# Kernel optimization log

Measured on AMD Instinct MI355X. Metric: run time of the kernel, lower is better.

Reference implementation:

```python
import jax, jax.numpy as jnp
import numpy as np

# DualAttention dims
D_MODEL = 1024
H_SA = 8          # self-attention heads
H_RA = 8          # relational-attention heads
TOTAL_H = H_SA + H_RA
HEAD_DIM = D_MODEL // TOTAL_H   # 64
KEY_DIM = HEAD_DIM              # 64
N_REL = 8
REL_PROJ = HEAD_DIM * H_RA // N_REL  # 64
B, S = 2, 2048


def apply_rope(x, cos, sin):
    # x: [b, s, h, d]; cos/sin: [s, d//2]. Pairs are (0,1),(2,3),... as in
    # llama-style apply_rotary_emb (reshape(..., -1, 2).unbind(-1)).
    xr, xi = x[..., 0::2], x[..., 1::2]
    c = cos[None, :, None, :]
    s_ = sin[None, :, None, :]
    out = jnp.stack([xr * c - xi * s_, xr * s_ + xi * c], axis=-1)
    return out.reshape(x.shape)


def setup_inputs() -> dict:
    key = jax.random.key(0)
    ks = jax.random.split(key, 16)
    def w(k, shape):
        return jax.random.normal(k, shape, jnp.float32) * 0.02
    x = jax.random.normal(ks[0], (B, S, D_MODEL), jnp.float32)
    symbols = jax.random.normal(ks[1], (B, S, D_MODEL), jnp.float32)
    # real RoPE tables
    pos = np.arange(S, dtype=np.float32)[:, None]
    inv = 1.0 / (10000.0 ** (np.arange(0, KEY_DIM, 2, dtype=np.float32) / KEY_DIM))
    ang = pos * inv[None, :]
    freqs_cos = jnp.asarray(np.cos(ang), jnp.float32)
    freqs_sin = jnp.asarray(np.sin(ang), jnp.float32)
    return dict(
        x=x, symbols=symbols, freqs_cos=freqs_cos, freqs_sin=freqs_sin,
        # self-attention branch (torch Linear weights: [out, in])
        wq_sa=w(ks[2], (H_SA * KEY_DIM, D_MODEL)),
        wk_sa=w(ks[3], (H_SA * KEY_DIM, D_MODEL)),
        wv_sa=w(ks[4], (H_SA * HEAD_DIM, D_MODEL)),
        wo_sa=w(ks[5], (H_SA * HEAD_DIM, H_SA * HEAD_DIM)),
        # relational-attention branch
        wq_attn=w(ks[6], (H_RA * KEY_DIM, D_MODEL)),
        wk_attn=w(ks[7], (H_RA * KEY_DIM, D_MODEL)),
        wq_rel=w(ks[8], (N_REL * REL_PROJ, D_MODEL)),
        wk_rel=w(ks[9], (N_REL * REL_PROJ, D_MODEL)),
        wr=w(ks[10], (H_RA, HEAD_DIM, N_REL)),
        wv_ra=w(ks[11], (H_RA * HEAD_DIM, D_MODEL)),
        wo_ra=w(ks[12], (H_RA * HEAD_DIM, H_RA * HEAD_DIM)),
    )


def reference(x, symbols, freqs_cos, freqs_sin,
              wq_sa, wk_sa, wv_sa, wo_sa,
              wq_attn, wk_attn, wq_rel, wk_rel, wr, wv_ra, wo_ra):
    b, s, _ = x.shape
    attn_scale = 1.0 / np.sqrt(HEAD_DIM).astype(np.float32)
    rel_scale = 1.0 / np.sqrt(REL_PROJ).astype(np.float32)
    causal = jnp.tril(jnp.ones((s, s), dtype=bool))
    neg = jnp.finfo(x.dtype).min

    def heads(t, h, d):
        return t.reshape(b, s, h, d)

    # ---- self-attention branch (causal SDPA with RoPE) ----
    q = apply_rope(heads(x @ wq_sa.T, H_SA, KEY_DIM), freqs_cos, freqs_sin)
    k = apply_rope(heads(x @ wk_sa.T, H_SA, KEY_DIM), freqs_cos, freqs_sin)
    v = heads(x @ wv_sa.T, H_SA, HEAD_DIM)
    scores = jnp.einsum('bihd,bjhd->bhij', q, k) * attn_scale
    a = jax.nn.softmax(jnp.where(causal, scores, neg), axis=-1)
    sa_out = jnp.einsum('bhij,bjhd->bihd', a, v).reshape(b, s, H_SA * HEAD_DIM) @ wo_sa.T

    # ---- relational-attention branch ----
    # attention scores (softmax selection), with RoPE
    qa = apply_rope(heads(x @ wq_attn.T, H_RA, KEY_DIM), freqs_cos, freqs_sin)
    ka = apply_rope(heads(x @ wk_attn.T, H_RA, KEY_DIM), freqs_cos, freqs_sin)
    ra_scores = jnp.einsum('bihd,bjhd->bhij', qa, ka) * attn_scale
    alpha = jax.nn.softmax(jnp.where(causal, ra_scores, neg), axis=-1)
    # relations r(x_i, x_j) in R^{N_REL} (identity rel_activation)
    qr = heads(x @ wq_rel.T, N_REL, REL_PROJ)
    kr = heads(x @ wk_rel.T, N_REL, REL_PROJ)
    rel = jnp.einsum('birp,bjrp->brij', qr, kr) * rel_scale  # [b, R, i, j]
    # symbol values: wv applied to retrieved symbols
    sv = heads(symbols @ wv_ra.T, H_RA, HEAD_DIM)
    attended_sym = jnp.einsum('bhij,bjhd->bihd', alpha, sv)          # [b, i, h, d]
    attended_rel = jnp.einsum('bhij,brij->bihr', alpha, rel)         # [b, i, h, R]
    rel_out = jnp.einsum('bihr,hdr->bihd', attended_rel, wr)
    ra_out = (attended_sym + rel_out).reshape(b, s, H_RA * HEAD_DIM) @ wo_ra.T

    # DualAttention: concat branch outputs along feature dim -> [b, s, d_model]
    return jnp.concatenate([sa_out, ra_out], axis=-1)
```

## Files before the change

kernel.cpp:

```cpp
#include <hip/hip_runtime.h>

#define B_   2
#define S_   2048
#define H_   8
#define D_   64
#define DM_  1024
#define PJ_  512
#define NT_  32
#define NTRI 528
#define NCHK 80

typedef short bf16x8 __attribute__((ext_vector_type(8)));
typedef float f32x4 __attribute__((ext_vector_type(4)));

__device__ __forceinline__ float bf2f(unsigned int u) {
  return __uint_as_float(u << 16);
}
__device__ __forceinline__ unsigned short f2bf(float f) {
  unsigned int u = __float_as_uint(f);
  u += 0x7fffu + ((u >> 16) & 1u);
  return (unsigned short)(u >> 16);
}

struct CvtJobs {
  const float*    src[12];
  unsigned short* dst[12];
  int             n4[12];
};

__global__ __launch_bounds__(256) void cvt_many(CvtJobs J) {
  const int j = blockIdx.y;
  const int i = blockIdx.x * 256 + threadIdx.x;
  if (i >= J.n4[j]) return;
  const float4 v = ((const float4*)J.src[j])[i];
  ushort4 o;
  o.x = f2bf(v.x); o.y = f2bf(v.y); o.z = f2bf(v.z); o.w = f2bf(v.w);
  ((ushort4*)J.dst[j])[i] = o;
}

template <int KD, typename CT>
__device__ __forceinline__
void gemm128_body(const unsigned short* __restrict__ A, int m0,
                  const unsigned short* __restrict__ Wb,
                  CT* __restrict__ Cb, int ldc,
                  unsigned short* As, unsigned short* Bs)
{
  const int tid = threadIdx.x;
  const int wv = tid >> 6, lane = tid & 63;
  const int r15 = lane & 15, quad = lane >> 4;
  const int wm = (wv >> 1) * 64, wn = (wv & 1) * 64;
  f32x4 acc[4][4];
#pragma unroll
  for (int i = 0; i < 4; ++i)
#pragma unroll
    for (int j = 0; j < 4; ++j) acc[i][j] = (f32x4){0.f, 0.f, 0.f, 0.f};

  const int srow = tid >> 1;
  const int sc2  = (tid & 1) * 2;
  const unsigned short* ga = A + (size_t)(m0 + srow) * KD + sc2 * 8;
  const unsigned short* gb = Wb + (size_t)srow * KD + sc2 * 8;
  unsigned short* la = As + srow * 40 + sc2 * 8;
  unsigned short* lb = Bs + srow * 40 + sc2 * 8;

  for (int kk = 0; kk < KD; kk += 32) {
    __syncthreads();
    const uint4 a0 = *(const uint4*)(ga + kk);
    const uint4 a1 = *(const uint4*)(ga + kk + 8);
    const uint4 b0 = *(const uint4*)(gb + kk);
    const uint4 b1 = *(const uint4*)(gb + kk + 8);
    *(uint4*)la       = a0;
    *(uint4*)(la + 8) = a1;
    *(uint4*)lb       = b0;
    *(uint4*)(lb + 8) = b1;
    __syncthreads();
    bf16x8 af[4], bf[4];
#pragma unroll
    for (int i = 0; i < 4; ++i)
      af[i] = *(const bf16x8*)(As + (wm + i * 16 + r15) * 40 + quad * 8);
#pragma unroll
    for (int j = 0; j < 4; ++j)
      bf[j] = *(const bf16x8*)(Bs + (wn + j * 16 + r15) * 40 + quad * 8);
#pragma unroll
    for (int i = 0; i < 4; ++i)
#pragma unroll
      for (int j = 0; j < 4; ++j)
        acc[i][j] = __builtin_amdgcn_mfma_f32_16x16x32_bf16(af[i], bf[j], acc[i][j], 0, 0, 0);
  }
#pragma unroll
  for (int i = 0; i < 4; ++i)
#pragma unroll
    for (int r = 0; r < 4; ++r) {
      CT* cp = Cb + (size_t)(wm + i * 16 + quad * 4 + r) * ldc + wn + r15;
#pragma unroll
      for (int j = 0; j < 4; ++j) {
        if constexpr (sizeof(CT) == 2) cp[j * 16] = f2bf(acc[i][j][r]);
        else                           cp[j * 16] = acc[i][j][r];
      }
    }
}

__global__ __launch_bounds__(256)
void proj_tiled(const unsigned short* __restrict__ XB,
                const unsigned short* __restrict__ SYB,
                const unsigned short* __restrict__ Wcat,
                unsigned short* __restrict__ Qbase,
                unsigned short* __restrict__ SV)
{
  __shared__ unsigned short As[128 * 40];
  __shared__ unsigned short Bs[128 * 40];
  const int m0 = blockIdx.x * 128;
  const int ny = blockIdx.y;
  const size_t NB = (size_t)B_ * S_ * PJ_;
  const unsigned short* A;
  const unsigned short* Wb;
  unsigned short* Cb;
  if (ny < 28) {
    const int n0 = ny * 128;
    A  = XB;
    Wb = Wcat + (size_t)n0 * DM_;
    Cb = Qbase + (size_t)(n0 >> 9) * NB + (size_t)m0 * PJ_ + (n0 & 511);
  } else {
    const int n0 = (ny - 28) * 128;
    A  = SYB;
    Wb = Wcat + (size_t)7 * PJ_ * DM_ + (size_t)n0 * DM_;
    Cb = SV + (size_t)m0 * PJ_ + n0;
  }
  gemm128_body<DM_, unsigned short>(A, m0, Wb, Cb, PJ_, As, Bs);
}

__global__ __launch_bounds__(256)
void out_tiled(const unsigned short* __restrict__ Asa,
               const unsigned short* __restrict__ Ara,
               const unsigned short* __restrict__ WOSA,
               const unsigned short* __restrict__ WORA,
               float* __restrict__ Out)
{
  __shared__ unsigned short As[128 * 40];
  __shared__ unsigned short Bs[64 * 40];
  const int m0 = blockIdx.x * 128;
  const int ny = blockIdx.y;
  const int n0 = (ny & 7) * 64;
  const unsigned short* A  = (ny < 8) ? Asa : Ara;
  const unsigned short* Wb = ((ny < 8) ? WOSA : WORA) + (size_t)n0 * PJ_;
  float* Cb = Out + (size_t)m0 * DM_ + ((ny < 8) ? 0 : 512) + n0;

  const int tid = threadIdx.x;
  const int wv = tid >> 6, lane = tid & 63;
  const int r15 = lane & 15, quad = lane >> 4;
  const int wm = wv * 32;
  f32x4 acc[2][4];
#pragma unroll
  for (int i = 0; i < 2; ++i)
#pragma unroll
    for (int j = 0; j < 4; ++j) acc[i][j] = (f32x4){0.f, 0.f, 0.f, 0.f};

  const int arow = tid >> 1, ac = (tid & 1) * 16;
  const int brow = tid >> 2, bc = (tid & 3) * 8;
  const unsigned short* ga = A + (size_t)(m0 + arow) * PJ_ + ac;
  const unsigned short* gb = Wb + (size_t)brow * PJ_ + bc;
  unsigned short* la = As + arow * 40 + ac;
  unsigned short* lb = Bs + brow * 40 + bc;

  for (int kk = 0; kk < PJ_; kk += 32) {
    __syncthreads();
    const uint4 a0 = *(const uint4*)(ga + kk);
    const uint4 a1 = *(const uint4*)(ga + kk + 8);
    const uint4 b0 = *(const uint4*)(gb + kk);
    *(uint4*)la       = a0;
    *(uint4*)(la + 8) = a1;
    *(uint4*)lb       = b0;
    __syncthreads();
    bf16x8 af[2], bf[4];
#pragma unroll
    for (int i = 0; i < 2; ++i)
      af[i] = *(const bf16x8*)(As + (wm + i * 16 + r15) * 40 + quad * 8);
#pragma unroll
    for (int j = 0; j < 4; ++j)
      bf[j] = *(const bf16x8*)(Bs + (j * 16 + r15) * 40 + quad * 8);
#pragma unroll
    for (int i = 0; i < 2; ++i)
#pragma unroll
      for (int j = 0; j < 4; ++j)
        acc[i][j] = __builtin_amdgcn_mfma_f32_16x16x32_bf16(af[i], bf[j], acc[i][j], 0, 0, 0);
  }
#pragma unroll
  for (int i = 0; i < 2; ++i)
#pragma unroll
    for (int r = 0; r < 4; ++r) {
      float* cp = Cb + (size_t)(wm + i * 16 + quad * 4 + r) * DM_ + r15;
#pragma unroll
      for (int j = 0; j < 4; ++j) cp[j * 16] = acc[i][j][r];
    }
}

__global__ __launch_bounds__(256)
void rel_gemm(const unsigned short* __restrict__ QRg, const unsigned short* __restrict__ KRg,
              unsigned short* __restrict__ RelCF)
{
  __shared__ unsigned short As[128 * 72];
  __shared__ unsigned short Bs[128 * 72];
  const int t = blockIdx.x;
  int I = 0;
  while ((I + 1) * (I + 2) / 2 <= t) ++I;
  const int J = t - I * (I + 1) / 2;
  const int rr = blockIdx.y & 7, b = blockIdx.y >> 3;
  const int tid = threadIdx.x;
  const int wv = tid >> 6, lane = tid & 63;
  const int r15 = lane & 15, quad = lane >> 4;

  const int srow = tid >> 1, c32 = (tid & 1) * 32;
  const unsigned short* ga = QRg + (size_t)(b * S_ + I * 128 + srow) * PJ_ + rr * 64 + c32;
  const unsigned short* gb = KRg + (size_t)(b * S_ + J * 128 + srow) * PJ_ + rr * 64 + c32;
  unsigned short* la = As + srow * 72 + c32;
  unsigned short* lb = Bs + srow * 72 + c32;
#pragma unroll
  for (int q = 0; q < 4; ++q) {
    *(uint4*)(la + q * 8) = *(const uint4*)(ga + q * 8);
    *(uint4*)(lb + q * 8) = *(const uint4*)(gb + q * 8);
  }
  __syncthreads();

  const int wm = (wv >> 1) * 64, wn = (wv & 1) * 64;
  const int it64 = 2 * I + (wv >> 1), jt64 = 2 * J + (wv & 1);
  if (jt64 > it64) return;
  f32x4 acc[4][4];
#pragma unroll
  for (int i = 0; i < 4; ++i)
#pragma unroll
    for (int j = 0; j < 4; ++j) acc[i][j] = (f32x4){0.f, 0.f, 0.f, 0.f};
#pragma unroll
  for (int k0 = 0; k0 < 2; ++k0) {
    bf16x8 af[4], bf[4];
#pragma unroll
    for (int i = 0; i < 4; ++i)
      af[i] = *(const bf16x8*)(As + (wm + i * 16 + r15) * 72 + quad * 8 + k0 * 32);
#pragma unroll
    for (int j = 0; j < 4; ++j)
      bf[j] = *(const bf16x8*)(Bs + (wn + j * 16 + r15) * 72 + quad * 8 + k0 * 32);
#pragma unroll
    for (int i = 0; i < 4; ++i)
#pragma unroll
      for (int j = 0; j < 4; ++j)
        acc[i][j] = __builtin_amdgcn_mfma_f32_16x16x32_bf16(af[i], bf[j], acc[i][j], 0, 0, 0);
  }
  unsigned short* out = RelCF + ((size_t)(b * 8 + rr) * NTRI + (size_t)it64 * (it64 + 1) / 2 + jt64) * 4096;
#pragma unroll
  for (int i = 0; i < 4; ++i) {
    unsigned short tmp[16];
#pragma unroll
    for (int j = 0; j < 4; ++j)
#pragma unroll
      for (int r = 0; r < 4; ++r)
        tmp[j * 4 + r] = f2bf(acc[i][j][r] * 0.125f);
    unsigned short* op = out + (size_t)(i * 64 + lane) * 16;
    *(uint4*)op       = *(const uint4*)tmp;
    *(uint4*)(op + 8) = *(const uint4*)(tmp + 8);
  }
}

__global__ __launch_bounds__(256)
void rope_kernel(unsigned short* Q, unsigned short* K,
                 unsigned short* QA, unsigned short* KA,
                 const float* __restrict__ fc,
                 const float* __restrict__ fs) {
  const int idx = blockIdx.x * 256 + threadIdx.x;
  const int t  = idx >> 20;
  const int r  = idx & 0xFFFFF;
  const int ci = r & 31;
  const int h  = (r >> 5) & 7;
  const int s  = (r >> 8) & 2047;
  const int b  = r >> 19;
  unsigned short* P = (t == 0) ? Q : (t == 1) ? K : (t == 2) ? QA : KA;
  const size_t off = ((size_t)(b * S_ + s)) * PJ_ + h * D_ + (ci << 1);
  const float xr = bf2f(P[off]);
  const float xi = bf2f(P[off + 1]);
  const float cs = fc[s * 32 + ci];
  const float sn = fs[s * 32 + ci];
  P[off]     = f2bf(xr * cs - xi * sn);
  P[off + 1] = f2bf(xr * sn + xi * cs);
}

__global__ __launch_bounds__(256)
void flash_part(const unsigned short* __restrict__ Qsa, const unsigned short* __restrict__ Ksa,
                const unsigned short* __restrict__ Vsa,
                const unsigned short* __restrict__ Qra, const unsigned short* __restrict__ Kra,
                const unsigned short* __restrict__ SVra,
                const unsigned short* __restrict__ RelCF,
                unsigned short* __restrict__ PoP, float* __restrict__ lP,
                float* __restrict__ arpP)
{
  __shared__ unsigned short Ks[2][64][72];
  __shared__ unsigned short Vt[2][64][72];
  __shared__ unsigned short Ps[64][72];
  const int x = blockIdx.x;
  int it, c;
  if (x < 8)       { it = x;                    c = 0; }
  else if (x < 24) { it = 8 + ((x - 8) >> 1);   c = (x - 8) & 1; }
  else if (x < 48) { it = 16 + (x - 24) / 3;    c = (x - 24) % 3; }
  else             { it = 24 + ((x - 48) >> 2); c = (x - 48) & 3; }
  const int j0 = c * 8;
  const int jend = (j0 + 8 < it + 1) ? (j0 + 8) : (it + 1);
  const bool ra = (blockIdx.y >= 8);
  const int h = blockIdx.y & 7;
  const int b = blockIdx.z;
  const int chunkId = (b * 16 + (int)blockIdx.y) * NCHK + x;
  const unsigned short* Qg = ra ? Qra : Qsa;
  const unsigned short* Kg = ra ? Kra : Ksa;
  const unsigned short* Vg = ra ? SVra : Vsa;
  const int tid = threadIdx.x;
  const int wv = tid >> 6, lane = tid & 63;
  const int r15 = lane & 15, quad = lane >> 4;
  const size_t bh = (size_t)b * S_ * PJ_ + (size_t)h * D_;
  const size_t relStride = (size_t)NTRI * 4096;

  const int kr0 = tid >> 3, kc0 = (tid & 7) << 3;
  const int kr1 = (tid + 256) >> 3;
  const unsigned short* kgp = Kg + bh + kc0;
  const unsigned short* vgp = Vg + bh + (size_t)lane * PJ_ + wv * 8;

  const unsigned short* qp = Qg + bh + (size_t)(it * 64 + wv * 16 + r15) * PJ_ + quad * 8;
  const bf16x8 aq0 = *(const bf16x8*)qp;
  const bf16x8 aq1 = *(const bf16x8*)(qp + 32);

  unsigned short one8[8];
#pragma unroll
  for (int i = 0; i < 8; ++i) one8[i] = 0x3F80;
  const bf16x8 ones = *(const bf16x8*)one8;

  f32x4 o_acc[4];
  f32x4 l_acc = {0.f, 0.f, 0.f, 0.f};
  float arp[4][8];
#pragma unroll
  for (int n = 0; n < 4; ++n) o_acc[n] = (f32x4){0.f, 0.f, 0.f, 0.f};
#pragma unroll
  for (int r = 0; r < 4; ++r)
#pragma unroll
    for (int rr = 0; rr < 8; ++rr) arp[r][rr] = 0.f;
  const int row0 = it * 64 + wv * 16 + quad * 4;
  const size_t relTileBase = (size_t)(b * 8) * NTRI * 4096
                           + (size_t)(it * (it + 1)) / 2 * 4096
                           + (size_t)(wv * 64 + lane) * 16;

  uint4 ka0, ka1, va0, va1;
  {
    const size_t jb = (size_t)j0 * 64 * PJ_;
    ka0 = *(const uint4*)(kgp + jb + (size_t)kr0 * PJ_);
    ka1 = *(const uint4*)(kgp + jb + (size_t)kr1 * PJ_);
    va0 = *(const uint4*)(vgp + jb);
    va1 = *(const uint4*)(vgp + jb + 32);
  }
  int p = 0;
  {
    *(uint4*)&Ks[0][kr0][kc0] = ka0;
    *(uint4*)&Ks[0][kr1][kc0] = ka1;
    unsigned short t8[8];
    *(uint4*)t8 = va0;
#pragma unroll
    for (int m = 0; m < 8; ++m) Vt[0][wv * 8 + m][lane] = t8[m];
    *(uint4*)t8 = va1;
#pragma unroll
    for (int m = 0; m < 8; ++m) Vt[0][wv * 8 + 32 + m][lane] = t8[m];
  }
  __syncthreads();

  for (int jt = j0; jt < jend; ++jt) {
    const bool more = (jt + 1 < jend);
    if (more) {
      const size_t jb = (size_t)(jt + 1) * 64 * PJ_;
      ka0 = *(const uint4*)(kgp + jb + (size_t)kr0 * PJ_);
      ka1 = *(const uint4*)(kgp + jb + (size_t)kr1 * PJ_);
      va0 = *(const uint4*)(vgp + jb);
      va1 = *(const uint4*)(vgp + jb + 32);
    }
    uint4 pre[8];
    const unsigned short* rtBase = RelCF + relTileBase + (size_t)jt * 4096;
    if (ra) {
      const unsigned short* rt = rtBase;
#pragma unroll
      for (int q = 0; q < 4; ++q) {
        pre[2 * q]     = *(const uint4*)rt;
        pre[2 * q + 1] = *(const uint4*)(rt + 8);
        rt += relStride;
      }
    }
    f32x4 s[4];
#pragma unroll
    for (int n = 0; n < 4; ++n) s[n] = (f32x4){0.f, 0.f, 0.f, 0.f};
#pragma unroll
    for (int k0 = 0; k0 < 2; ++k0) {
      const bf16x8 af = k0 ? aq1 : aq0;
#pragma unroll
      for (int n = 0; n < 4; ++n) {
        const bf16x8 bf = *(const bf16x8*)&Ks[p][n * 16 + r15][quad * 8 + k0 * 32];
        s[n] = __builtin_amdgcn_mfma_f32_16x16x32_bf16(af, bf, s[n], 0, 0, 0);
      }
    }
    if (jt == it) {
#pragma unroll
      for (int n = 0; n < 4; ++n)
#pragma unroll
        for (int r = 0; r < 4; ++r) {
          const bool ok = (jt * 64 + n * 16 + r15 <= row0 + r);
          s[n][r] = ok ? __expf(s[n][r] * 0.125f - 4.0f) : 0.f;
        }
    } else {
#pragma unroll
      for (int n = 0; n < 4; ++n)
#pragma unroll
        for (int r = 0; r < 4; ++r)
          s[n][r] = __expf(s[n][r] * 0.125f - 4.0f);
    }
#pragma unroll
    for (int n = 0; n < 4; ++n)
#pragma unroll
      for (int r = 0; r < 4; ++r)
        Ps[wv * 16 + quad * 4 + r][n * 16 + r15] = f2bf(s[n][r]);
    if (ra) {
      const unsigned short* rt2 = rtBase + 4 * relStride;
#pragma unroll
      for (int rr = 0; rr < 8; ++rr) {
        unsigned short rv[16];
        if (rr < 4) {
          *(uint4*)rv       = pre[2 * rr];
          *(uint4*)(rv + 8) = pre[2 * rr + 1];
        } else {
          *(uint4*)rv       = *(const uint4*)rt2;
          *(uint4*)(rv + 8) = *(const uint4*)(rt2 + 8);
          rt2 += relStride;
        }
#pragma unroll
        for (int n = 0; n < 4; ++n)
#pragma unroll
          for (int r = 0; r < 4; ++r)
            arp[r][rr] += s[n][r] * bf2f(rv[n * 4 + r]);
      }
    }
#pragma unroll
    for (int k0 = 0; k0 < 2; ++k0) {
      const bf16x8 pf = *(const bf16x8*)&Ps[wv * 16 + r15][quad * 8 + k0 * 32];
#pragma unroll
      for (int n = 0; n < 4; ++n) {
        const bf16x8 vf = *(const bf16x8*)&Vt[p][n * 16 + r15][quad * 8 + k0 * 32];
        o_acc[n] = __builtin_amdgcn_mfma_f32_16x16x32_bf16(pf, vf, o_acc[n], 0, 0, 0);
      }
      l_acc = __builtin_amdgcn_mfma_f32_16x16x32_bf16(pf, ones, l_acc, 0, 0, 0);
    }
    if (more) {
      const int q = p ^ 1;
      *(uint4*)&Ks[q][kr0][kc0] = ka0;
      *(uint4*)&Ks[q][kr1][kc0] = ka1;
      unsigned short t8[8];
      *(uint4*)t8 = va0;
#pragma unroll
      for (int m = 0; m < 8; ++m) Vt[q][wv * 8 + m][lane] = t8[m];
      *(uint4*)t8 = va1;
#pragma unroll
      for (int m = 0; m < 8; ++m) Vt[q][wv * 8 + 32 + m][lane] = t8[m];
      __syncthreads();
      p = q;
    }
  }
  unsigned short* po = PoP + (size_t)chunkId * 4096;
#pragma unroll
  for (int n = 0; n < 4; ++n)
#pragma unroll
    for (int r = 0; r < 4; ++r)
      po[(wv * 16 + quad * 4 + r) * 64 + n * 16 + r15] = f2bf(o_acc[n][r]);
  if (r15 == 0) {
#pragma unroll
    for (int r = 0; r < 4; ++r)
      lP[(size_t)chunkId * 64 + wv * 16 + quad * 4 + r] = l_acc[r];
  }
  if (ra) {
#pragma unroll
    for (int r = 0; r < 4; ++r)
#pragma unroll
      for (int rr = 0; rr < 8; ++rr)
#pragma unroll
        for (int o = 1; o < 16; o <<= 1)
          arp[r][rr] += __shfl_xor(arp[r][rr], o);
    if (r15 == 0) {
#pragma unroll
      for (int r = 0; r < 4; ++r) {
        float* ap = arpP + (size_t)chunkId * 512 + (wv * 16 + quad * 4 + r) * 8;
#pragma unroll
        for (int rr = 0; rr < 8; ++rr) ap[rr] = arp[r][rr];
      }
    }
  }
}

__global__ __launch_bounds__(256)
void flash_merge(const unsigned short* __restrict__ PoP, const float* __restrict__ lP,
                 const float* __restrict__ arpP, const float* __restrict__ wrF,
                 unsigned short* __restrict__ Osa, unsigned short* __restrict__ Ora)
{
  const int it = blockIdx.x;
  const int hh = blockIdx.y;
  const int b  = blockIdx.z;
  const bool ra = (hh >= 8);
  const int h = hh & 7;
  const int nc = it / 8 + 1;
  int cb;
  if (it < 8)       cb = it;
  else if (it < 16) cb = 8 + 2 * (it - 8);
  else if (it < 24) cb = 24 + 3 * (it - 16);
  else              cb = 48 + 4 * (it - 24);
  const int cid0 = (b * 16 + hh) * NCHK + cb;
  const int tid = threadIdx.x;
  const int row = tid >> 2;
  const int cg  = tid & 3;

  float L = 0.f;
  for (int c = 0; c < nc; ++c) L += lP[(size_t)(cid0 + c) * 64 + row];
  const float inv = 1.f / L;

  float o[16];
#pragma unroll
  for (int k = 0; k < 16; ++k) o[k] = 0.f;
  for (int c = 0; c < nc; ++c) {
    const unsigned short* pp = PoP + (size_t)(cid0 + c) * 4096 + row * 64 + cg * 16;
    unsigned short t[16];
    *(uint4*)t       = *(const uint4*)pp;
    *(uint4*)(t + 8) = *(const uint4*)(pp + 8);
#pragma unroll
    for (int k = 0; k < 16; ++k) o[k] += bf2f(t[k]);
  }
  if (ra) {
    float A[8];
#pragma unroll
    for (int rr = 0; rr < 8; ++rr) A[rr] = 0.f;
    for (int c = 0; c < nc; ++c) {
      const float* ap = arpP + (size_t)(cid0 + c) * 512 + row * 8;
#pragma unroll
      for (int rr = 0; rr < 8; ++rr) A[rr] += ap[rr];
    }
#pragma unroll
    for (int k = 0; k < 16; ++k) {
      const float* wp = wrF + ((size_t)h * 64 + cg * 16 + k) * 8;
      float ro = 0.f;
#pragma unroll
      for (int rr = 0; rr < 8; ++rr) ro += A[rr] * wp[rr];
      o[k] += ro;
    }
  }
  const size_t bh = (size_t)b * S_ * PJ_ + (size_t)h * D_;
  unsigned short* op = (ra ? Ora : Osa) + bh + (size_t)(it * 64 + row) * PJ_ + cg * 16;
#pragma unroll
  for (int k = 0; k < 16; ++k) op[k] = f2bf(o[k] * inv);
}

extern "C" void kernel_launch(void* const* d_in, const int* in_sizes, int n_in,
                              void* d_out, int out_size, void* d_ws, size_t ws_size,
                              hipStream_t stream)
{
  (void)in_sizes; (void)n_in; (void)out_size; (void)ws_size;
  const float* x    = (const float*)d_in[0];
  const float* sym  = (const float*)d_in[1];
  const float* fc   = (const float*)d_in[2];
  const float* fs   = (const float*)d_in[3];
  const float* wqsa = (const float*)d_in[4];
  const float* wksa = (const float*)d_in[5];
  const float* wvsa = (const float*)d_in[6];
  const float* wosa = (const float*)d_in[7];
  const float* wqat = (const float*)d_in[8];
  const float* wkat = (const float*)d_in[9];
  const float* wqre = (const float*)d_in[10];
  const float* wkre = (const float*)d_in[11];
  const float* wr   = (const float*)d_in[12];
  const float* wvra = (const float*)d_in[13];
  const float* wora = (const float*)d_in[14];

  unsigned short* wsb = (unsigned short*)d_ws;
  const size_t NX = (size_t)B_ * S_ * DM_;
  const size_t NB = (size_t)B_ * S_ * PJ_;
  const size_t NW = (size_t)PJ_ * DM_;
  const size_t NO = (size_t)PJ_ * PJ_;
  const size_t NR = (size_t)B_ * 8 * NTRI * 4096;
  const size_t NCH = (size_t)B_ * 16 * NCHK;

  size_t off = 0;
  unsigned short* XB   = wsb + off; off += NX;
  unsigned short* SYB  = wsb + off; off += NX;
  unsigned short* WB[8];
  for (int i = 0; i < 8; ++i) { WB[i] = wsb + off; off += NW; }
  unsigned short* WOSA = wsb + off; off += NO;
  unsigned short* WORA = wsb + off; off += NO;
  unsigned short* Q    = wsb + off; off += NB;
  unsigned short* K    = wsb + off; off += NB;
  unsigned short* V    = wsb + off; off += NB;
  unsigned short* QA   = wsb + off; off += NB;
  unsigned short* KA   = wsb + off; off += NB;
  unsigned short* QR   = wsb + off; off += NB;
  unsigned short* KR   = wsb + off; off += NB;
  unsigned short* SV   = wsb + off; off += NB;
  unsigned short* Asa  = wsb + off; off += NB;
  unsigned short* Ara  = wsb + off; off += NB;
  unsigned short* RelCF = wsb + off; off += NR;
  unsigned short* PoP  = XB;
  float* lP   = (float*)(wsb + off); off += NCH * 64 * 2;
  float* arpP = (float*)(wsb + off); off += NCH * 512 * 2;

  CvtJobs cj;
  cj.src[0]  = x;    cj.dst[0]  = XB;    cj.n4[0]  = (int)(NX / 4);
  cj.src[1]  = sym;  cj.dst[1]  = SYB;   cj.n4[1]  = (int)(NX / 4);
  cj.src[2]  = wqsa; cj.dst[2]  = WB[0]; cj.n4[2]  = (int)(NW / 4);
  cj.src[3]  = wksa; cj.dst[3]  = WB[1]; cj.n4[3]  = (int)(NW / 4);
  cj.src[4]  = wvsa; cj.dst[4]  = WB[2]; cj.n4[4]  = (int)(NW / 4);
  cj.src[5]  = wqat; cj.dst[5]  = WB[3]; cj.n4[5]  = (int)(NW / 4);
  cj.src[6]  = wkat; cj.dst[6]  = WB[4]; cj.n4[6]  = (int)(NW / 4);
  cj.src[7]  = wqre; cj.dst[7]  = WB[5]; cj.n4[7]  = (int)(NW / 4);
  cj.src[8]  = wkre; cj.dst[8]  = WB[6]; cj.n4[8]  = (int)(NW / 4);
  cj.src[9]  = wvra; cj.dst[9]  = WB[7]; cj.n4[9]  = (int)(NW / 4);
  cj.src[10] = wosa; cj.dst[10] = WOSA;  cj.n4[10] = (int)(NO / 4);
  cj.src[11] = wora; cj.dst[11] = WORA;  cj.n4[11] = (int)(NO / 4);
  cvt_many<<<dim3(4096, 12), dim3(256), 0, stream>>>(cj);

  proj_tiled<<<dim3(32, 32), dim3(256), 0, stream>>>(XB, SYB, WB[0], Q, SV);
  rope_kernel<<<dim3(16384), dim3(256), 0, stream>>>(Q, K, QA, KA, fc, fs);
  rel_gemm<<<dim3(136, 16), dim3(256), 0, stream>>>(QR, KR, RelCF);
  flash_part<<<dim3(NCHK, 16, B_), dim3(256), 0, stream>>>(
      Q, K, V, QA, KA, SV, RelCF, PoP, lP, arpP);
  flash_merge<<<dim3(NT_, 16, B_), dim3(256), 0, stream>>>(
      PoP, lP, arpP, wr, Asa, Ara);
  out_tiled<<<dim3(32, 16), dim3(256), 0, stream>>>(Asa, Ara, WOSA, WORA, (float*)d_out);
}
```

Before: 337.7 us.

## Use direct global-to-LDS loads in projection GEMM and single-buffer flash K/V

The projection GEMM now stages A and B tiles with global_load_lds, which moves data from global memory straight into LDS without passing through registers. It uses a packed 32-wide row with an XOR swizzle in place of the padded 40-wide rows. The flash-attention kernel drops its double-buffered K/V shared arrays for single buffers with 68-element padding, adding an extra barrier before each overwrite. This cuts LDS use, which may raise occupancy, but it serialises loads against compute in the flash loop.

Result: no change. 332.1 us (-1.7%).

```diff
diff --git a/kernel.cpp b/kernel.cpp
--- a/kernel.cpp
+++ b/kernel.cpp
@@ -22,6 +22,12 @@
   return (unsigned short)(u >> 16);
 }
 
+__device__ __forceinline__ void glds16(const unsigned short* g, unsigned short* l) {
+  __builtin_amdgcn_global_load_lds(
+      (const __attribute__((address_space(1))) void*)g,
+      (__attribute__((address_space(3))) void*)l, 16, 0, 0);
+}
+
 struct CvtJobs {
   const float*    src[12];
   unsigned short* dst[12];
@@ -38,11 +44,10 @@
   ((ushort4*)J.dst[j])[i] = o;
 }
 
-template <int KD, typename CT>
 __device__ __forceinline__
-void gemm128_body(const unsigned short* __restrict__ A, int m0,
+void gemm128_glds(const unsigned short* __restrict__ A, int m0,
                   const unsigned short* __restrict__ Wb,
-                  CT* __restrict__ Cb, int ldc,
+                  unsigned short* __restrict__ Cb, int ldc, int KD,
                   unsigned short* As, unsigned short* Bs)
 {
   const int tid = threadIdx.x;
@@ -55,31 +60,32 @@
 #pragma unroll
     for (int j = 0; j < 4; ++j) acc[i][j] = (f32x4){0.f, 0.f, 0.f, 0.f};
 
-  const int srow = tid >> 1;
-  const int sc2  = (tid & 1) * 2;
-  const unsigned short* ga = A + (size_t)(m0 + srow) * KD + sc2 * 8;
-  const unsigned short* gb = Wb + (size_t)srow * KD + sc2 * 8;
-  unsigned short* la = As + srow * 40 + sc2 * 8;
-  unsigned short* lb = Bs + srow * 40 + sc2 * 8;
+  const int srow = wv * 16 + (lane >> 2);
+  const int scol = ((lane & 3) ^ ((lane >> 3) & 3)) * 8;
+  const unsigned short* gaA0 = A + (size_t)(m0 + srow) * KD + scol;
+  const unsigned short* gaA1 = gaA0 + (size_t)64 * KD;
+  const unsigned short* gaB0 = Wb + (size_t)srow * KD + scol;
+  const unsigned short* gaB1 = gaB0 + (size_t)64 * KD;
+  unsigned short* ldsA0 = As + wv * 512;
+  unsigned short* ldsA1 = As + 2048 + wv * 512;
+  unsigned short* ldsB0 = Bs + wv * 512;
+  unsigned short* ldsB1 = Bs + 2048 + wv * 512;
+  const int rxor = (r15 >> 1) & 3;
 
   for (int kk = 0; kk < KD; kk += 32) {
     __syncthreads();
-    const uint4 a0 = *(const uint4*)(ga + kk);
-    const uint4 a1 = *(const uint4*)(ga + kk + 8);
-    const uint4 b0 = *(const uint4*)(gb + kk);
-    const uint4 b1 = *(const uint4*)(gb + kk + 8);
-    *(uint4*)la       = a0;
-    *(uint4*)(la + 8) = a1;
-    *(uint4*)lb       = b0;
-    *(uint4*)(lb + 8) = b1;
+    glds16(gaA0 + kk, ldsA0);
+    glds16(gaA1 + kk, ldsA1);
+    glds16(gaB0 + kk, ldsB0);
+    glds16(gaB1 + kk, ldsB1);
     __syncthreads();
     bf16x8 af[4], bf[4];
 #pragma unroll
     for (int i = 0; i < 4; ++i)
-      af[i] = *(const bf16x8*)(As + (wm + i * 16 + r15) * 40 + quad * 8);
+      af[i] = *(const bf16x8*)(As + (wm + i * 16 + r15) * 32 + ((quad ^ rxor) << 3));
 #pragma unroll
     for (int j = 0; j < 4; ++j)
-      bf[j] = *(const bf16x8*)(Bs + (wn + j * 16 + r15) * 40 + quad * 8);
+      bf[j] = *(const bf16x8*)(Bs + (wn + j * 16 + r15) * 32 + ((quad ^ rxor) << 3));
 #pragma unroll
     for (int i = 0; i < 4; ++i)
 #pragma unroll
@@ -90,12 +96,9 @@
   for (int i = 0; i < 4; ++i)
 #pragma unroll
     for (int r = 0; r < 4; ++r) {
-      CT* cp = Cb + (size_t)(wm + i * 16 + quad * 4 + r) * ldc + wn + r15;
-#pragma unroll
-      for (int j = 0; j < 4; ++j) {
-        if constexpr (sizeof(CT) == 2) cp[j * 16] = f2bf(acc[i][j][r]);
-        else                           cp[j * 16] = acc[i][j][r];
-      }
+      unsigned short* cp = Cb + (size_t)(wm + i * 16 + quad * 4 + r) * ldc + wn + r15;
+#pragma unroll
+      for (int j = 0; j < 4; ++j) cp[j * 16] = f2bf(acc[i][j][r]);
     }
 }
 
@@ -106,8 +109,8 @@
                 unsigned short* __restrict__ Qbase,
                 unsigned short* __restrict__ SV)
 {
-  __shared__ unsigned short As[128 * 40];
-  __shared__ unsigned short Bs[128 * 40];
+  __shared__ unsigned short As[128 * 32];
+  __shared__ unsigned short Bs[128 * 32];
   const int m0 = blockIdx.x * 128;
   const int ny = blockIdx.y;
   const size_t NB = (size_t)B_ * S_ * PJ_;
@@ -125,7 +128,7 @@
     Wb = Wcat + (size_t)7 * PJ_ * DM_ + (size_t)n0 * DM_;
     Cb = SV + (size_t)m0 * PJ_ + n0;
   }
-  gemm128_body<DM_, unsigned short>(A, m0, Wb, Cb, PJ_, As, Bs);
+  gemm128_glds(A, m0, Wb, Cb, PJ_, DM_, As, Bs);
 }
 
 __global__ __launch_bounds__(256)
@@ -289,9 +292,9 @@
                 unsigned short* __restrict__ PoP, float* __restrict__ lP,
                 float* __restrict__ arpP)
 {
-  __shared__ unsigned short Ks[2][64][72];
-  __shared__ unsigned short Vt[2][64][72];
-  __shared__ unsigned short Ps[64][72];
+  __shared__ unsigned short Ks[64][68];
+  __shared__ unsigned short Vt[64][68];
+  __shared__ unsigned short Ps[64][68];
   const int x = blockIdx.x;
   int it, c;
   if (x < 8)       { it = x;                    c = 0; }
@@ -349,17 +352,16 @@
     va0 = *(const uint4*)(vgp + jb);
     va1 = *(const uint4*)(vgp + jb + 32);
   }
-  int p = 0;
   {
-    *(uint4*)&Ks[0][kr0][kc0] = ka0;
-    *(uint4*)&Ks[0][kr1][kc0] = ka1;
+    *(uint4*)&Ks[kr0][kc0] = ka0;
+    *(uint4*)&Ks[kr1][kc0] = ka1;
     unsigned short t8[8];
     *(uint4*)t8 = va0;
 #pragma unroll
-    for (int m = 0; m < 8; ++m) Vt[0][wv * 8 + m][lane] = t8[m];
+    for (int m = 0; m < 8; ++m) Vt[wv * 8 + m][lane] = t8[m];
     *(uint4*)t8 = va1;
 #pragma unroll
-    for (int m = 0; m < 8; ++m) Vt[0][wv * 8 + 32 + m][lane] = t8[m];
+    for (int m = 0; m < 8; ++m) Vt[wv * 8 + 32 + m][lane] = t8[m];
   }
   __syncthreads();
 
@@ -391,7 +393,7 @@
       const bf16x8 af = k0 ? aq1 : aq0;
 #pragma unroll
       for (int n = 0; n < 4; ++n) {
-        const bf16x8 bf = *(const bf16x8*)&Ks[p][n * 16 + r15][quad * 8 + k0 * 32];
+        const bf16x8 bf = *(const bf16x8*)&Ks[n * 16 + r15][quad * 8 + k0 * 32];
         s[n] = __builtin_amdgcn_mfma_f32_16x16x32_bf16(af, bf, s[n], 0, 0, 0);
       }
     }
@@ -440,24 +442,23 @@
       const bf16x8 pf = *(const bf16x8*)&Ps[wv * 16 + r15][quad * 8 + k0 * 32];
 #pragma unroll
       for (int n = 0; n < 4; ++n) {
-        const bf16x8 vf = *(const bf16x8*)&Vt[p][n * 16 + r15][quad * 8 + k0 * 32];
+        const bf16x8 vf = *(const bf16x8*)&Vt[n * 16 + r15][quad * 8 + k0 * 32];
         o_acc[n] = __builtin_amdgcn_mfma_f32_16x16x32_bf16(pf, vf, o_acc[n], 0, 0, 0);
       }
       l_acc = __builtin_amdgcn_mfma_f32_16x16x32_bf16(pf, ones, l_acc, 0, 0, 0);
     }
     if (more) {
-      const int q = p ^ 1;
-      *(uint4*)&Ks[q][kr0][kc0] = ka0;
-      *(uint4*)&Ks[q][kr1][kc0] = ka1;
+      __syncthreads();
+      *(uint4*)&Ks[kr0][kc0] = ka0;
+      *(uint4*)&Ks[kr1][kc0] = ka1;
       unsigned short t8[8];
       *(uint4*)t8 = va0;
 #pragma unroll
-      for (int m = 0; m < 8; ++m) Vt[q][wv * 8 + m][lane] = t8[m];
+      for (int m = 0; m < 8; ++m) Vt[wv * 8 + m][lane] = t8[m];
       *(uint4*)t8 = va1;
 #pragma unroll
-      for (int m = 0; m < 8; ++m) Vt[q][wv * 8 + 32 + m][lane] = t8[m];
+      for (int m = 0; m < 8; ++m) Vt[wv * 8 + 32 + m][lane] = t8[m];
       __syncthreads();
-      p = q;
     }
   }
   unsigned short* po = PoP + (size_t)chunkId * 4096;
```
